# Optimization experiments

Measured on AMD Instinct MI355X. Metric: run time of the kernel, lower is better.

## Reference

```python
import jax, jax.numpy as jnp
import numpy as np

D_MODEL = 1024
NUM_HEADS = 16
HEAD_DIM = D_MODEL // NUM_HEADS  # 64
SCALE = HEAD_DIM ** -0.5
BIAS_LEN = 128  # min(max_seq_len=512, 128)
ROPE_BASE = 10000.0
LN_EPS = 1e-5


def setup_inputs() -> dict:
    key = jax.random.key(0)
    ks = jax.random.split(key, 8)
    B, Lq, Lkv = 8, 512, 512
    return {
        "decoder_hidden": jax.random.normal(ks[0], (B, Lq, D_MODEL), jnp.float32),
        "encoder_output": jax.random.normal(ks[1], (B, Lkv, D_MODEL), jnp.float32),
        "Wqkv": jax.random.normal(ks[2], (3 * D_MODEL, D_MODEL), jnp.float32) * 0.02,
        "Wout": jax.random.normal(ks[3], (D_MODEL, D_MODEL), jnp.float32) * 0.02,
        "b_out": jnp.zeros((D_MODEL,), jnp.float32),
        "Wgate": jax.random.normal(ks[4], (D_MODEL, D_MODEL), jnp.float32) * 0.02,
        "b_gate": jnp.zeros((D_MODEL,), jnp.float32),
        "gamma": jnp.ones((D_MODEL,), jnp.float32),
        "beta": jnp.zeros((D_MODEL,), jnp.float32),
    }


def _layernorm(x, gamma, beta):
    mu = jnp.mean(x, axis=-1, keepdims=True)
    var = jnp.mean(jnp.square(x - mu), axis=-1, keepdims=True)
    return (x - mu) * jax.lax.rsqrt(var + LN_EPS) * gamma + beta


def _rope(x, cos, sin):
    # x: [B, H, L, HEAD_DIM]; cos/sin: [L, HEAD_DIM//2]
    half = HEAD_DIM // 2
    c = cos[None, None, :, :]
    s = sin[None, None, :, :]
    x_even, x_odd = x[..., :half], x[..., half:]
    return jnp.concatenate([x_even * c - x_odd * s, x_even * s + x_odd * c], axis=-1)


def _temporal_bias(L_q, L_kv):
    pos = jnp.arange(BIAS_LEN, dtype=jnp.float32)
    dist = jnp.abs(pos[None, :] - pos[:, None])  # [128,128]
    bias = jnp.exp(-dist * 0.1) - dist * 0.05
    if L_q <= BIAS_LEN and L_kv <= BIAS_LEN:
        return bias[:L_q, :L_kv]
    # bilinear interpolation (align_corners=False / half-pixel) fallback
    return jax.image.resize(bias, (L_q, L_kv), method="bilinear")


def reference(decoder_hidden, encoder_output, Wqkv, Wout, b_out, Wgate, b_gate, gamma, beta):
    B, L_q, _ = decoder_hidden.shape
    L_kv = encoder_output.shape[1]
    residual = decoder_hidden

    q_in = _layernorm(decoder_hidden, gamma, beta)
    kv_in = _layernorm(encoder_output, gamma, beta)

    q = q_in @ Wqkv[:D_MODEL].T
    k = kv_in @ Wqkv[D_MODEL:2 * D_MODEL].T
    v = kv_in @ Wqkv[2 * D_MODEL:].T

    q = q.reshape(B, L_q, NUM_HEADS, HEAD_DIM).transpose(0, 2, 1, 3)
    k = k.reshape(B, L_kv, NUM_HEADS, HEAD_DIM).transpose(0, 2, 1, 3)
    v = v.reshape(B, L_kv, NUM_HEADS, HEAD_DIM).transpose(0, 2, 1, 3)

    # rotary embedding over max(L_q, L_kv) positions
    L = max(L_q, L_kv)
    inv_freq = 1.0 / ROPE_BASE ** (jnp.arange(0, HEAD_DIM, 2, dtype=jnp.float32) / HEAD_DIM)
    freqs = jnp.arange(L, dtype=jnp.float32)[:, None] * inv_freq[None, :]  # [L, HEAD_DIM//2]
    cos, sin = jnp.cos(freqs), jnp.sin(freqs)
    q = _rope(q, cos[:L_q], sin[:L_q])
    k = _rope(k, cos[:L_kv], sin[:L_kv])

    scores = jnp.einsum("bhqd,bhkd->bhqk", q, k) * SCALE
    scores = scores + _temporal_bias(L_q, L_kv)[None, None, :, :]

    attn = jax.nn.softmax(scores, axis=-1)
    attended = jnp.einsum("bhqk,bhkd->bhqd", attn, v)
    attended = attended.transpose(0, 2, 1, 3).reshape(B, L_q, D_MODEL)
    attended = attended @ Wout.T + b_out

    gate = jax.nn.sigmoid(attended @ Wgate.T + b_gate)
    output = gate * attended + (1.0 - gate) * residual
    return output
```

## Files before the change

kernel.cpp:

```cpp
#include <hip/hip_runtime.h>
#include <hip/hip_bf16.h>

#define D_MODEL 1024
#define NHEADS 16
#define HDIM 64
#define BATCH 8
#define SEQ 512
#define NROWS 4096
#define SCALE 0.125f
#define LN_EPS 1e-5f

typedef __attribute__((ext_vector_type(8))) short bf16x8;
typedef __attribute__((ext_vector_type(4))) float f32x4;
typedef __attribute__((ext_vector_type(8))) unsigned short u16x8;

static __device__ __forceinline__ float bf2f(unsigned short u) {
    return __uint_as_float(((unsigned int)u) << 16);
}
static __device__ __forceinline__ unsigned short f2bf(float f) {
    unsigned int x = __float_as_uint(f);
    unsigned int r = (x + 0x7fffu + ((x >> 16) & 1u)) >> 16;
    return (unsigned short)r;
}

#define GLOAD16(gp, lp)                                                        \
    __builtin_amdgcn_global_load_lds(                                          \
        (const __attribute__((address_space(1))) void*)(gp),                   \
        (__attribute__((address_space(3))) void*)(lp), 16, 0, 0)

#define VMW(n) asm volatile("s_waitcnt vmcnt(" #n ")" ::: "memory")
#define RBAR() __builtin_amdgcn_s_barrier()

static __device__ __forceinline__ float bias128(int a, int b) {
    float d = fabsf((float)(a - b));
    return expf(-d * 0.1f) - d * 0.05f;
}

__global__ void prep_kernel(const float* __restrict__ dec, const float* __restrict__ enc,
                            const float* __restrict__ gamma, const float* __restrict__ beta,
                            const float* __restrict__ Wqkv,
                            const float* __restrict__ Wout, const float* __restrict__ Wgate,
                            unsigned short* __restrict__ q_ln, unsigned short* __restrict__ kv_ln,
                            float* __restrict__ bias, unsigned short* __restrict__ Wqkv_bf,
                            unsigned short* __restrict__ Wout_bf, unsigned short* __restrict__ Wgate_bf) {
    int blk = blockIdx.x;
    int t = threadIdx.x;
    if (blk >= 6144) {
        int idx = (blk - 6144) * 256 + t;
        const float* src; unsigned short* dst; int off;
        if (idx < 262144) { src = Wout; dst = Wout_bf; off = idx; }
        else              { src = Wgate; dst = Wgate_bf; off = idx - 262144; }
        float4 v = ((const float4*)src)[off];
        ushort4 u;
        u.x = f2bf(v.x); u.y = f2bf(v.y); u.z = f2bf(v.z); u.w = f2bf(v.w);
        ((ushort4*)dst)[off] = u;
        return;
    }
    if (blk >= 3072) {
        int idx = (blk - 3072) * 256 + t;
        float4 v = ((const float4*)Wqkv)[idx];
        ushort4 u;
        u.x = f2bf(v.x); u.y = f2bf(v.y); u.z = f2bf(v.z); u.w = f2bf(v.w);
        ((ushort4*)Wqkv_bf)[idx] = u;
        return;
    }
    if (blk >= 2048) {
        int idx = (blk - 2048) * 256 + t;
        int qi = idx >> 9, kj = idx & 511;
        float fq = (qi + 0.5f) * 0.25f - 0.5f;
        float fk = (kj + 0.5f) * 0.25f - 0.5f;
        int iq = (int)floorf(fq); float tq = fq - (float)iq;
        int ik = (int)floorf(fk); float tk = fk - (float)ik;
        int iq0 = min(max(iq, 0), 127), iq1 = min(max(iq + 1, 0), 127);
        int ik0 = min(max(ik, 0), 127), ik1 = min(max(ik + 1, 0), 127);
        float v = (1.f - tq) * ((1.f - tk) * bias128(iq0, ik0) + tk * bias128(iq0, ik1))
                +        tq  * ((1.f - tk) * bias128(iq1, ik0) + tk * bias128(iq1, ik1));
        bias[idx] = v;
        return;
    }
    int row = blk * 4 + (t >> 6);
    int lane = t & 63;
    const float* src = (row < NROWS) ? dec + (size_t)row * D_MODEL
                                     : enc + (size_t)(row - NROWS) * D_MODEL;
    unsigned short* dst = (row < NROWS) ? q_ln + (size_t)row * D_MODEL
                                        : kv_ln + (size_t)(row - NROWS) * D_MODEL;
    float4 x0 = ((const float4*)src)[lane];
    float4 x1 = ((const float4*)src)[lane + 64];
    float4 x2 = ((const float4*)src)[lane + 128];
    float4 x3 = ((const float4*)src)[lane + 192];
    float s  = x0.x + x0.y + x0.z + x0.w + x1.x + x1.y + x1.z + x1.w
             + x2.x + x2.y + x2.z + x2.w + x3.x + x3.y + x3.z + x3.w;
    float ss = x0.x * x0.x + x0.y * x0.y + x0.z * x0.z + x0.w * x0.w
             + x1.x * x1.x + x1.y * x1.y + x1.z * x1.z + x1.w * x1.w
             + x2.x * x2.x + x2.y * x2.y + x2.z * x2.z + x2.w * x2.w
             + x3.x * x3.x + x3.y * x3.y + x3.z * x3.z + x3.w * x3.w;
    #pragma unroll
    for (int off = 32; off > 0; off >>= 1) {
        s  += __shfl_down(s, off);
        ss += __shfl_down(ss, off);
    }
    s  = __shfl(s, 0);
    ss = __shfl(ss, 0);
    float mu  = s * (1.0f / 1024.0f);
    float var = ss * (1.0f / 1024.0f) - mu * mu;
    float rstd = rsqrtf(var + LN_EPS);
    #pragma unroll
    for (int j = 0; j < 4; ++j) {
        float4 xv = (j == 0) ? x0 : (j == 1) ? x1 : (j == 2) ? x2 : x3;
        float4 g  = ((const float4*)gamma)[lane + j * 64];
        float4 bb = ((const float4*)beta)[lane + j * 64];
        ushort4 u;
        u.x = f2bf((xv.x - mu) * rstd * g.x + bb.x);
        u.y = f2bf((xv.y - mu) * rstd * g.y + bb.y);
        u.z = f2bf((xv.z - mu) * rstd * g.z + bb.z);
        u.w = f2bf((xv.w - mu) * rstd * g.w + bb.w);
        ((ushort4*)dst)[lane + j * 64] = u;
    }
}

__global__ void convert_og(const float* __restrict__ Wout, const float* __restrict__ Wgate,
                           unsigned short* __restrict__ Wout_bf, unsigned short* __restrict__ Wgate_bf) {
    int idx = blockIdx.x * 256 + threadIdx.x;
    const float* src; unsigned short* dst; int off;
    if (idx < 262144) { src = (const float*)Wout; dst = Wout_bf; off = idx; }
    else              { src = (const float*)Wgate; dst = Wgate_bf; off = idx - 262144; }
    float4 v = ((const float4*)src)[off];
    ushort4 u;
    u.x = f2bf(v.x); u.y = f2bf(v.y); u.z = f2bf(v.z); u.w = f2bf(v.w);
    ((ushort4*)dst)[off] = u;
}

#define CSTR 136

#define MF(a, b, d) __builtin_amdgcn_mfma_f32_16x16x32_bf16((a), (b), (d), 0, 0, 0)

union alignas(16) SmemQS {
    struct { unsigned short A[64 * 64]; unsigned short B[128 * 64]; } ab;
    unsigned short C[64 * CSTR];
    unsigned short Ct[128 * 72];
};

#define QKH(pA, pB, kh)                                                        \
    {                                                                          \
        int pofs = (((kh) * 4 + quad) ^ x7) * 8;                               \
        const unsigned short* Ar_ = (pA) + (wr * 32 + c) * 64 + pofs;          \
        const unsigned short* Br_ = (pB) + (wc * 64 + c) * 64 + pofs;          \
        bf16x8 f0 = *(const bf16x8*)(Ar_);                                     \
        bf16x8 f1 = *(const bf16x8*)(Ar_ + 1024);                              \
        bf16x8 g0 = *(const bf16x8*)(Br_);                                     \
        bf16x8 g1 = *(const bf16x8*)(Br_ + 1024);                              \
        bf16x8 g2 = *(const bf16x8*)(Br_ + 2048);                              \
        bf16x8 g3 = *(const bf16x8*)(Br_ + 3072);                              \
        c00 = MF(f0, g0, c00); c01 = MF(f0, g1, c01); c02 = MF(f0, g2, c02); c03 = MF(f0, g3, c03); \
        c10 = MF(f1, g0, c10); c11 = MF(f1, g1, c11); c12 = MF(f1, g2, c12); c13 = MF(f1, g3, c13); \
    }

#define QROPE_REG(i, reg, A0, A1, A2, A3)                                      \
    {                                                                          \
        int mloc = wr * 32 + (i) * 16 + quad * 4 + (reg);                      \
        int crow = mloc * CSTR + wc * 64;                                      \
        float fl = (float)((rt * 64 + mloc) & 511);                            \
        float aa0 = fl * inv0, aa1 = fl * inv1;                                \
        float c0 = cosf(aa0), s0 = sinf(aa0);                                  \
        float c1 = cosf(aa1), s1 = sinf(aa1);                                  \
        float e0 = A0[(reg)], o0 = A2[(reg)];                                  \
        float e1 = A1[(reg)], o1 = A3[(reg)];                                  \
        smemq.C[crow + c]      = f2bf(e0 * c0 - o0 * s0);                      \
        smemq.C[crow + 32 + c] = f2bf(e0 * s0 + o0 * c0);                      \
        smemq.C[crow + 16 + c] = f2bf(e1 * c1 - o1 * s1);                      \
        smemq.C[crow + 48 + c] = f2bf(e1 * s1 + o1 * c1);                      \
    }
#define QROPE_ROW(i, A0, A1, A2, A3)                                           \
    QROPE_REG(i, 0, A0, A1, A2, A3) QROPE_REG(i, 1, A0, A1, A2, A3)            \
    QROPE_REG(i, 2, A0, A1, A2, A3) QROPE_REG(i, 3, A0, A1, A2, A3)

#define QVSECT_REG(i, j, reg, Acc)                                             \
    smemq.Ct[(wc * 64 + (j) * 16 + c) * 72 + (wr * 32 + (i) * 16 + quad * 4 + (reg))] = f2bf(Acc[(reg)]);
#define QVSECT_TILE(i, j, Acc)                                                 \
    QVSECT_REG(i, j, 0, Acc) QVSECT_REG(i, j, 1, Acc)                          \
    QVSECT_REG(i, j, 2, Acc) QVSECT_REG(i, j, 3, Acc)

__global__ __launch_bounds__(256, 6)
void qkv_gemm_mfma(const unsigned short* __restrict__ q_ln,
                   const unsigned short* __restrict__ kv_ln,
                   const unsigned short* __restrict__ Wb,
                   unsigned short* __restrict__ qo,
                   unsigned short* __restrict__ ko,
                   unsigned short* __restrict__ vo) {
    int bid = blockIdx.x;
    int wg = (bid & 7) * 192 + (bid >> 3);
    int st = wg >> 5, in = wg & 31;
    int stc = st >> 4, str = st & 15;
    int ct = stc * 8 + (in & 7);
    int rt = str * 4 + (in >> 3);
    int n0 = ct * 128;
    int section = stc;
    const unsigned short* A = (section == 0) ? q_ln : kv_ln;

    __shared__ SmemQS smemq;
    unsigned short* As2 = smemq.ab.A;
    unsigned short* Bs2 = smemq.ab.B;
    int tid = threadIdx.x;
    int wave = tid >> 6, lane = tid & 63, quad = lane >> 4, c = lane & 15;
    int wr = wave >> 1, wc = wave & 1;
    int x7 = c & 7;

    int soff = (tid >> 3) * 1024 + (((tid & 7) ^ ((tid >> 3) & 7)) * 8);
    const unsigned short* Ab = A + (size_t)(rt * 64) * 1024 + soff;
    const unsigned short* Bb = Wb + (size_t)n0 * 1024 + soff;
    int stW = wave * 512;

    f32x4 c00 = (f32x4)0.f, c01 = (f32x4)0.f, c02 = (f32x4)0.f, c03 = (f32x4)0.f;
    f32x4 c10 = (f32x4)0.f, c11 = (f32x4)0.f, c12 = (f32x4)0.f, c13 = (f32x4)0.f;

    for (int kt = 0; kt < 16; ++kt) {
        int k0 = kt * 64;
        __syncthreads();
        GLOAD16(Ab + k0,          As2 + stW);
        GLOAD16(Ab + 32768 + k0,  As2 + stW + 2048);
        GLOAD16(Bb + k0,          Bs2 + stW);
        GLOAD16(Bb + 32768 + k0,  Bs2 + stW + 2048);
        GLOAD16(Bb + 65536 + k0,  Bs2 + stW + 4096);
        GLOAD16(Bb + 98304 + k0,  Bs2 + stW + 6144);
        __syncthreads();
        QKH(As2, Bs2, 0)
        QKH(As2, Bs2, 1)
    }

    __syncthreads();

    if (section == 2) {
        QVSECT_TILE(0, 0, c00) QVSECT_TILE(0, 1, c01) QVSECT_TILE(0, 2, c02) QVSECT_TILE(0, 3, c03)
        QVSECT_TILE(1, 0, c10) QVSECT_TILE(1, 1, c11) QVSECT_TILE(1, 2, c12) QVSECT_TILE(1, 3, c13)
        __syncthreads();
        int dr = tid >> 1, hh = tid & 1;
        int h = ((n0 & 1023) >> 6) + (dr >> 6);
        int d = dr & 63;
        int mmb = rt * 64;
        int bb = mmb >> 9, ll0 = mmb & 511;
        unsigned short* orow = vo + (((size_t)bb * NHEADS + h) * HDIM + d) * SEQ + ll0 + hh * 32;
        const unsigned short* csrc = &smemq.Ct[dr * 72 + hh * 32];
        #pragma unroll
        for (int kc = 0; kc < 4; ++kc)
            *(u16x8*)(orow + kc * 8) = *(const u16x8*)(csrc + kc * 8);
        return;
    }

    float inv0 = expf(-0.2878231366f * (float)c);
    float inv1 = expf(-0.2878231366f * (float)(16 + c));
    QROPE_ROW(0, c00, c01, c02, c03)
    QROPE_ROW(1, c10, c11, c12, c13)
    __syncthreads();

    unsigned short* outp = (section == 0) ? qo : ko;
    int rr = tid >> 2;
    int ch = (tid >> 1) & 1;
    int sub = tid & 1;
    int mm = rt * 64 + rr;
    int bb = mm >> 9, ll = mm & 511;
    int h = ((n0 & 1023) >> 6) + ch;
    unsigned short* orow = outp + (((size_t)bb * NHEADS + h) * SEQ + ll) * HDIM + sub * 32;
    const unsigned short* csrc = &smemq.C[rr * CSTR + ch * 64 + sub * 32];
    #pragma unroll
    for (int kc = 0; kc < 4; ++kc)
        *(u16x8*)(orow + kc * 8) = *(const u16x8*)(csrc + kc * 8);
}

struct alignas(16) SmemOG {
    unsigned short A[64 * 128];
    unsigned short B[64 * 128];
};

#define OG_KH(kh)                                                              \
    {                                                                          \
        int pofs = (((kh) * 4 + quad) ^ c) * 8;                                \
        const unsigned short* Ar_ = smemog.A + (wr * 32 + c) * 128 + pofs;     \
        const unsigned short* Br_ = smemog.B + (wc * 32 + c) * 128 + pofs;     \
        bf16x8 f0 = *(const bf16x8*)(Ar_);                                     \
        bf16x8 f1 = *(const bf16x8*)(Ar_ + 2048);                              \
        bf16x8 g0 = *(const bf16x8*)(Br_);                                     \
        bf16x8 g1 = *(const bf16x8*)(Br_ + 2048);                              \
        c00 = MF(f0, g0, c00); c01 = MF(f0, g1, c01);                          \
        c10 = MF(f1, g0, c10); c11 = MF(f1, g1, c11);                          \
    }

#define OG_BODY(Aptr, Bptr)                                                    \
    int bid = blockIdx.x;                                         \
    int wg = (bid & 7) * 128 + (bid >> 3);      \
    int ct = wg & 15, rt = wg >> 4;                                            \
    int tid = threadIdx.x;                                                     \
    int wave = tid >> 6, lane = tid & 63, quad = lane >> 4, c = lane & 15;     \
    int wr = wave >> 1, wc = wave & 1;                                         \
     \
    int soff = (tid >> 4) * 1024 + (((tid & 15) ^ ((tid >> 4) & 15)) * 8);     \
    const unsigned short* Ab = (Aptr) + (size_t)(rt * 64) * 1024 + soff;       \
    const unsigned short* Bb = (Bptr) + (size_t)(ct * 64) * 1024 + soff;       \
    int stW = wave * 512;                                                      \
    f32x4 c00 = (f32x4)0.f, c01 = (f32x4)0.f;                                  \
    f32x4 c10 = (f32x4)0.f, c11 = (f32x4)0.f;                                  \
    for (int kt = 0; kt < 8; ++kt) {                                           \
        int k0 = kt * 128;                                                     \
        __syncthreads();                                                       \
        GLOAD16(Ab + k0,          smemog.A + stW);                             \
        GLOAD16(Ab + 16384 + k0,  smemog.A + stW + 2048);                      \
        GLOAD16(Ab + 32768 + k0,  smemog.A + stW + 4096);                      \
        GLOAD16(Ab + 49152 + k0,  smemog.A + stW + 6144);                      \
        GLOAD16(Bb + k0,          smemog.B + stW);                             \
        GLOAD16(Bb + 16384 + k0,  smemog.B + stW + 2048);                      \
        GLOAD16(Bb + 32768 + k0,  smemog.B + stW + 4096);                      \
        GLOAD16(Bb + 49152 + k0,  smemog.B + stW + 6144);                      \
        __syncthreads();                                                       \
        OG_KH(0)                                                               \
        OG_KH(1)                                                               \
        OG_KH(2)                                                               \
        OG_KH(3)                                                               \
    }

#define O1_REG(mb, reg, n, Acc)                                                \
    t_bf[(size_t)((mb) + (reg)) * 1024 + (n)] = f2bf(Acc[(reg)] + bo);
#define O1_TILE(i, j, Acc)                                                     \
    {                                                                          \
        int n = ct * 64 + wc * 32 + (j) * 16 + c;                              \
        float bo = b_out[n];                                                   \
        int mb = rt * 64 + wr * 32 + (i) * 16 + quad * 4;                      \
        O1_REG(mb, 0, n, Acc) O1_REG(mb, 1, n, Acc)                            \
        O1_REG(mb, 2, n, Acc) O1_REG(mb, 3, n, Acc)                            \
    }

__global__ __launch_bounds__(256, 4)
void out_gemm1_mfma(const unsigned short* __restrict__ att,
                    const unsigned short* __restrict__ Wob,
                    const float* __restrict__ b_out,
                    unsigned short* __restrict__ t_bf) {
    __shared__ SmemOG smemog;
    OG_BODY(att, Wob)
    O1_TILE(0, 0, c00) O1_TILE(0, 1, c01)
    O1_TILE(1, 0, c10) O1_TILE(1, 1, c11)
}

#define O2_REG(mb, reg, n, Acc)                                                \
    {                                                                          \
        float gz = Acc[(reg)] + bg;                                            \
        float g = 1.0f / (1.0f + expf(-gz));                                   \
        size_t idx = (size_t)((mb) + (reg)) * 1024 + (n);                      \
        float tv = bf2f(t_bf[idx]);                                            \
        float rv = residual[idx];                                              \
        out[idx] = g * tv + (1.0f - g) * rv;                                   \
    }
#define O2_TILE(i, j, Acc)                                                     \
    {                                                                          \
        int n = ct * 64 + wc * 32 + (j) * 16 + c;                              \
        float bg = b_gate[n];                                                  \
        int mb = rt * 64 + wr * 32 + (i) * 16 + quad * 4;                      \
        O2_REG(mb, 0, n, Acc) O2_REG(mb, 1, n, Acc)                            \
        O2_REG(mb, 2, n, Acc) O2_REG(mb, 3, n, Acc)                            \
    }

__global__ __launch_bounds__(256, 4)
void out_gemm2_mfma(const unsigned short* __restrict__ t_bf,
                    const unsigned short* __restrict__ Wgb,
                    const float* __restrict__ b_gate,
                    const float* __restrict__ residual,
                    float* __restrict__ out) {
    __shared__ SmemOG smemog;
    OG_BODY(t_bf, Wgb)
    O2_TILE(0, 0, c00) O2_TILE(0, 1, c01)
    O2_TILE(1, 0, c10) O2_TILE(1, 1, c11)
}

#define KSTR 72

static __device__ __forceinline__ void attn_step(
    const unsigned short* __restrict__ KsB, const unsigned short* __restrict__ VsB,
    int kv0, const float* __restrict__ bias, unsigned short* __restrict__ Ps,
    int q0, int wb, int quad, int c, int p0, int p1,
    bf16x8 aq0, bf16x8 aq1, f32x4 (&oacc)[4], float (&lrow)[4])
{
    f32x4 sacc[4];
    #pragma unroll
    for (int nt = 0; nt < 4; ++nt) {
        const unsigned short* kbase = &KsB[(nt * 16 + c) * 64];
        bf16x8 b0 = *(const bf16x8*)(kbase + p0);
        bf16x8 b1 = *(const bf16x8*)(kbase + p1);
        f32x4 a = (f32x4)0.f;
        a = __builtin_amdgcn_mfma_f32_16x16x32_bf16(aq0, b0, a, 0, 0, 0);
        a = __builtin_amdgcn_mfma_f32_16x16x32_bf16(aq1, b1, a, 0, 0, 0);
        sacc[nt] = a;
    }
    const float* bbase = bias + (size_t)(q0 + wb + quad * 4) * 512 + kv0 + c;
    float tsum[4];
    #pragma unroll
    for (int r = 0; r < 4; ++r) tsum[r] = 0.f;
    #pragma unroll
    for (int nt = 0; nt < 4; ++nt)
        #pragma unroll
        for (int r = 0; r < 4; ++r) {
            float p = __expf(sacc[nt][r] * SCALE + bbase[(size_t)r * 512 + nt * 16]);
            tsum[r] += p;
            Ps[(wb + quad * 4 + r) * KSTR + nt * 16 + c] = f2bf(p);
        }
    #pragma unroll
    for (int r = 0; r < 4; ++r) {
        float t = tsum[r];
        t += __shfl_xor(t, 1);
        t += __shfl_xor(t, 2);
        t += __shfl_xor(t, 4);
        t += __shfl_xor(t, 8);
        lrow[r] += t;
    }
    bf16x8 pb0 = *(const bf16x8*)&Ps[(wb + c) * KSTR + quad * 8];
    bf16x8 pb1 = *(const bf16x8*)&Ps[(wb + c) * KSTR + 32 + quad * 8];
    #pragma unroll
    for (int t = 0; t < 4; ++t) {
        const unsigned short* vbase = &VsB[(t * 16 + c) * 64];
        bf16x8 a0 = *(const bf16x8*)(vbase + p0);
        bf16x8 a1 = *(const bf16x8*)(vbase + p1);
        oacc[t] = __builtin_amdgcn_mfma_f32_16x16x32_bf16(a0, pb0, oacc[t], 0, 0, 0);
        oacc[t] = __builtin_amdgcn_mfma_f32_16x16x32_bf16(a1, pb1, oacc[t], 0, 0, 0);
    }
}

#define ASTAGE(BUF, kvt)                                                       \
    GLOAD16(kgb + (size_t)((kvt) * 64) * HDIM, Ks[BUF] + wave * 512);          \
    GLOAD16(vgb + (kvt) * 64, Vs[BUF] + wave * 512);

__global__ __launch_bounds__(512)
void attn_kernel(const unsigned short* __restrict__ q,
                 const unsigned short* __restrict__ k,
                 const unsigned short* __restrict__ vt,
                 const float* __restrict__ bias,
                 unsigned short* __restrict__ attended) {
    int bid = blockIdx.x;
    int qt = bid >> 7;
    int hb = bid & 127;
    int h = hb >> 3;
    int b = hb & 7;
    __shared__ unsigned short Ks[2][64 * 64];
    __shared__ unsigned short Vs[2][64 * 64];
    __shared__ unsigned short Ps[128 * KSTR];
    __shared__ float lf[128];

    int tid = threadIdx.x;
    int wave = tid >> 6, lane = tid & 63;
    int quad = lane >> 4, c = lane & 15;
    int wb = wave * 16;
    size_t headbase = (((size_t)b * NHEADS + h) * SEQ) * HDIM;
    int q0 = qt * 128;

    const unsigned short* qrow = q + headbase + (size_t)(q0 + wb + c) * HDIM;
    bf16x8 aq0 = *(const bf16x8*)(qrow + quad * 8);
    bf16x8 aq1 = *(const bf16x8*)(qrow + 32 + quad * 8);

    int srow = wave * 8 + (lane >> 3);
    int schunk = (lane & 7) ^ (srow & 7);
    const unsigned short* kgb = k + headbase + (size_t)srow * HDIM + schunk * 8;
    const unsigned short* vgb = vt + headbase + (size_t)srow * SEQ + schunk * 8;
    int x7 = c & 7;
    int p0 = (quad ^ x7) * 8;
    int p1 = ((4 + quad) ^ x7) * 8;

    f32x4 oacc[4];
    #pragma unroll
    for (int t = 0; t < 4; ++t) oacc[t] = (f32x4)0.f;
    float lrow[4];
    #pragma unroll
    for (int r = 0; r < 4; ++r) lrow[r] = 0.f;

    ASTAGE(0, 0)
    ASTAGE(1, 1)
    VMW(2); RBAR();
    for (int kt2 = 0; kt2 < 4; ++kt2) {
        attn_step(Ks[0], Vs[0], (kt2 * 2) * 64, bias, Ps,
                  q0, wb, quad, c, p0, p1, aq0, aq1, oacc, lrow);
        RBAR();
        if (kt2 < 3) { ASTAGE(0, kt2 * 2 + 2) VMW(2); }
        else         { VMW(0); }
        RBAR();
        attn_step(Ks[1], Vs[1], (kt2 * 2 + 1) * 64, bias, Ps,
                  q0, wb, quad, c, p0, p1, aq0, aq1, oacc, lrow);
        RBAR();
        if (kt2 < 3) { ASTAGE(1, kt2 * 2 + 3) VMW(2); }
        RBAR();
    }

    if (c == 0) {
        f32x4 lv;
        lv[0] = lrow[0]; lv[1] = lrow[1]; lv[2] = lrow[2]; lv[3] = lrow[3];
        *(f32x4*)&lf[wb + quad * 4] = lv;
    }
    float invl = 1.0f / lf[wb + c];
    unsigned short* drow = attended + ((size_t)b * SEQ + (q0 + wb + c)) * D_MODEL + h * HDIM;
    #pragma unroll
    for (int t = 0; t < 4; ++t) {
        ushort4 o;
        o.x = f2bf(oacc[t][0] * invl);
        o.y = f2bf(oacc[t][1] * invl);
        o.z = f2bf(oacc[t][2] * invl);
        o.w = f2bf(oacc[t][3] * invl);
        *(ushort4*)(drow + t * 16 + quad * 4) = o;
    }
}

extern "C" void kernel_launch(void* const* d_in, const int* in_sizes, int n_in,
                              void* d_out, int out_size, void* d_ws, size_t ws_size,
                              hipStream_t stream) {
    const float* dec    = (const float*)d_in[0];
    const float* enc    = (const float*)d_in[1];
    const float* Wqkv   = (const float*)d_in[2];
    const float* Wout   = (const float*)d_in[3];
    const float* b_out  = (const float*)d_in[4];
    const float* Wgate  = (const float*)d_in[5];
    const float* b_gate = (const float*)d_in[6];
    const float* gamma  = (const float*)d_in[7];
    const float* beta   = (const float*)d_in[8];
    float* out = (float*)d_out;

    char* ws = (char*)d_ws;
    const size_t MB = 1024 * 1024;
    unsigned short* q_ln    = (unsigned short*)(ws + 0 * MB);
    unsigned short* kv_ln   = (unsigned short*)(ws + 8 * MB);
    unsigned short* qb      = (unsigned short*)(ws + 16 * MB);
    unsigned short* kb      = (unsigned short*)(ws + 24 * MB);
    unsigned short* vb      = (unsigned short*)(ws + 32 * MB);
    unsigned short* Wqkv_bf = (unsigned short*)(ws + 40 * MB);
    float*          bias    = (float*)(ws + 46 * MB);
    unsigned short* att     = (unsigned short*)(ws + 0 * MB);
    unsigned short* t_bf    = (unsigned short*)(ws + 24 * MB);

    bool hoist = (ws_size >= 51 * MB);
    unsigned short* Wout_bf  = (unsigned short*)(ws + (hoist ? 47 * MB : 32 * MB));
    unsigned short* Wgate_bf = (unsigned short*)(ws + (hoist ? 49 * MB : 34 * MB));

    prep_kernel<<<hoist ? 8192 : 6144, 256, 0, stream>>>(
        dec, enc, gamma, beta, Wqkv, Wout, Wgate,
        q_ln, kv_ln, bias, Wqkv_bf, Wout_bf, Wgate_bf);
    qkv_gemm_mfma<<<1536, 256, 0, stream>>>(q_ln, kv_ln, Wqkv_bf, qb, kb, vb);
    attn_kernel<<<512, 512, 0, stream>>>(qb, kb, vb, bias, att);
    if (!hoist)
        convert_og<<<2048, 256, 0, stream>>>(Wout, Wgate, Wout_bf, Wgate_bf);
    out_gemm1_mfma<<<1024, 256, 0, stream>>>(att, Wout_bf, b_out, t_bf);
    out_gemm2_mfma<<<1024, 256, 0, stream>>>(t_bf, Wgate_bf, b_gate, dec, out);
}
```

Before: 202.8 us.

## Fold Wout into gate weight to fuse both output GEMMs into one kernel

Computes a combined weight Wgate·Wout and bias Wgate·b_out+b_gate on the device each call, attached as extra blocks to the prep and QKV GEMM launches. A single fused output kernel then computes att·Wout and att·Wcomb together and applies the gate epilogue. This removes the intermediate t_bf round trip and one kernel launch. In exchange it adds a per-call 1024^3 weight GEMM, and rounding the combined weight to bf16 slightly changes numerics. The new path only runs when the workspace is at least 56 MB, otherwise the old two-GEMM path is used.

```diff
diff --git a/kernel.cpp b/kernel.cpp
--- a/kernel.cpp
+++ b/kernel.cpp
@@ -40,11 +40,45 @@
                             const float* __restrict__ gamma, const float* __restrict__ beta,
                             const float* __restrict__ Wqkv,
                             const float* __restrict__ Wout, const float* __restrict__ Wgate,
+                            const float* __restrict__ b_out, const float* __restrict__ b_gate,
                             unsigned short* __restrict__ q_ln, unsigned short* __restrict__ kv_ln,
                             float* __restrict__ bias, unsigned short* __restrict__ Wqkv_bf,
-                            unsigned short* __restrict__ Wout_bf, unsigned short* __restrict__ Wgate_bf) {
+                            unsigned short* __restrict__ Wout_bf, unsigned short* __restrict__ Wgate_bf,
+                            unsigned short* __restrict__ WoutT_bf, float* __restrict__ bias2) {
     int blk = blockIdx.x;
     int t = threadIdx.x;
+    __shared__ unsigned short T[64 * 72];
+    if (blk >= 8448) {
+        int n = (blk - 8448) * 256 + t;
+        float acc = 0.f;
+        const float4* wg4 = (const float4*)(Wgate + (size_t)n * 1024);
+        const float4* bo4 = (const float4*)b_out;
+        for (int k = 0; k < 256; ++k) {
+            float4 w = wg4[k]; float4 b = bo4[k];
+            acc += w.x * b.x + w.y * b.y + w.z * b.z + w.w * b.w;
+        }
+        bias2[n] = acc + b_gate[n];
+        return;
+    }
+    if (blk >= 8192) {
+        int tb = blk - 8192;
+        int tr = tb >> 4, tc = tb & 15;
+        int r = t >> 2, q4 = (t & 3) * 16;
+        const float* src = Wout + (size_t)(tr * 64 + r) * 1024 + tc * 64 + q4;
+        #pragma unroll
+        for (int p = 0; p < 4; ++p) {
+            float4 v = ((const float4*)src)[p];
+            T[(q4 + p * 4 + 0) * 72 + r] = f2bf(v.x);
+            T[(q4 + p * 4 + 1) * 72 + r] = f2bf(v.y);
+            T[(q4 + p * 4 + 2) * 72 + r] = f2bf(v.z);
+            T[(q4 + p * 4 + 3) * 72 + r] = f2bf(v.w);
+        }
+        __syncthreads();
+        unsigned short* dst = WoutT_bf + (size_t)(tc * 64 + r) * 1024 + tr * 64 + q4;
+        *(u16x8*)(dst)     = *(const u16x8*)&T[r * 72 + q4];
+        *(u16x8*)(dst + 8) = *(const u16x8*)&T[r * 72 + q4 + 8];
+        return;
+    }
     if (blk >= 6144) {
         int idx = (blk - 6144) * 256 + t;
         const float* src; unsigned short* dst; int off;
@@ -180,22 +214,48 @@
     QVSECT_REG(i, j, 0, Acc) QVSECT_REG(i, j, 1, Acc)                          \
     QVSECT_REG(i, j, 2, Acc) QVSECT_REG(i, j, 3, Acc)
 
+#define WC_TILE(i, j, Acc)                                                     \
+    {                                                                          \
+        int n_ = ct * 128 + wc * 64 + (j) * 16 + c;                            \
+        int m_ = rt * 64 + wr * 32 + (i) * 16 + quad * 4;                      \
+        Wcomb_bf[(size_t)(m_ + 0) * 1024 + n_] = f2bf(Acc[0]);                 \
+        Wcomb_bf[(size_t)(m_ + 1) * 1024 + n_] = f2bf(Acc[1]);                 \
+        Wcomb_bf[(size_t)(m_ + 2) * 1024 + n_] = f2bf(Acc[2]);                 \
+        Wcomb_bf[(size_t)(m_ + 3) * 1024 + n_] = f2bf(Acc[3]);                 \
+    }
+
 __global__ __launch_bounds__(256, 6)
 void qkv_gemm_mfma(const unsigned short* __restrict__ q_ln,
                    const unsigned short* __restrict__ kv_ln,
                    const unsigned short* __restrict__ Wb,
                    unsigned short* __restrict__ qo,
                    unsigned short* __restrict__ ko,
-                   unsigned short* __restrict__ vo) {
+                   unsigned short* __restrict__ vo,
+                   const unsigned short* __restrict__ Wgate_bf,
+                   const unsigned short* __restrict__ WoutT_bf,
+                   unsigned short* __restrict__ Wcomb_bf,
+                   int nwc) {
     int bid = blockIdx.x;
-    int wg = (bid & 7) * 192 + (bid >> 3);
-    int st = wg >> 5, in = wg & 31;
-    int stc = st >> 4, str = st & 15;
-    int ct = stc * 8 + (in & 7);
-    int rt = str * 4 + (in >> 3);
-    int n0 = ct * 128;
-    int section = stc;
-    const unsigned short* A = (section == 0) ? q_ln : kv_ln;
+    int section, ct, rt, n0;
+    const unsigned short *A, *B;
+    if (bid < nwc) {
+        section = 3;
+        rt = bid >> 3;
+        ct = bid & 7;
+        n0 = ct * 128;
+        A = Wgate_bf; B = WoutT_bf;
+    } else {
+        int b2 = bid - nwc;
+        int wg = (b2 & 7) * 192 + (b2 >> 3);
+        int st = wg >> 5, in = wg & 31;
+        int stc = st >> 4, str = st & 15;
+        ct = stc * 8 + (in & 7);
+        rt = str * 4 + (in >> 3);
+        n0 = ct * 128;
+        section = stc;
+        A = (section == 0) ? q_ln : kv_ln;
+        B = Wb;
+    }
 
     __shared__ SmemQS smemq;
     unsigned short* As2 = smemq.ab.A;
@@ -207,7 +267,7 @@
 
     int soff = (tid >> 3) * 1024 + (((tid & 7) ^ ((tid >> 3) & 7)) * 8);
     const unsigned short* Ab = A + (size_t)(rt * 64) * 1024 + soff;
-    const unsigned short* Bb = Wb + (size_t)n0 * 1024 + soff;
+    const unsigned short* Bb = B + (size_t)n0 * 1024 + soff;
     int stW = wave * 512;
 
     f32x4 c00 = (f32x4)0.f, c01 = (f32x4)0.f, c02 = (f32x4)0.f, c03 = (f32x4)0.f;
@@ -228,6 +288,12 @@
     }
 
     __syncthreads();
+
+    if (section == 3) {
+        WC_TILE(0, 0, c00) WC_TILE(0, 1, c01) WC_TILE(0, 2, c02) WC_TILE(0, 3, c03)
+        WC_TILE(1, 0, c10) WC_TILE(1, 1, c11) WC_TILE(1, 2, c12) WC_TILE(1, 3, c13)
+        return;
+    }
 
     if (section == 2) {
         QVSECT_TILE(0, 0, c00) QVSECT_TILE(0, 1, c01) QVSECT_TILE(0, 2, c02) QVSECT_TILE(0, 3, c03)
@@ -266,6 +332,85 @@
         *(u16x8*)(orow + kc * 8) = *(const u16x8*)(csrc + kc * 8);
 }
 
+struct alignas(16) SmemF {
+    unsigned short A[64 * 64];
+    unsigned short B1[64 * 64];
+    unsigned short B2[64 * 64];
+};
+
+#define FUS_KH(kh)                                                             \
+    {                                                                          \
+        int pofs = (((kh) * 4 + quad) ^ x7) * 8;                               \
+        const unsigned short* Ar_  = smf.A  + (wr * 32 + c) * 64 + pofs;       \
+        const unsigned short* B1r_ = smf.B1 + (wc * 32 + c) * 64 + pofs;       \
+        const unsigned short* B2r_ = smf.B2 + (wc * 32 + c) * 64 + pofs;       \
+        bf16x8 f0 = *(const bf16x8*)(B1r_ - B1r_ + Ar_);                       \
+        bf16x8 f1 = *(const bf16x8*)(Ar_ + 1024);                              \
+        bf16x8 g0 = *(const bf16x8*)(B1r_);                                    \
+        bf16x8 g1 = *(const bf16x8*)(B1r_ + 1024);                             \
+        bf16x8 h0 = *(const bf16x8*)(B2r_);                                    \
+        bf16x8 h1 = *(const bf16x8*)(B2r_ + 1024);                             \
+        c00 = MF(f0, g0, c00); c01 = MF(f0, g1, c01);                          \
+        c10 = MF(f1, g0, c10); c11 = MF(f1, g1, c11);                          \
+        d00 = MF(f0, h0, d00); d01 = MF(f0, h1, d01);                          \
+        d10 = MF(f1, h0, d10); d11 = MF(f1, h1, d11);                          \
+    }
+
+#define FO_TILE(i, j, CA, DA)                                                  \
+    {                                                                          \
+        int n = ct * 64 + wc * 32 + (j) * 16 + c;                              \
+        float bo = b_out[n];                                                   \
+        float b2v = bias2[n];                                                  \
+        int mb = rt * 64 + wr * 32 + (i) * 16 + quad * 4;                      \
+        _Pragma("unroll")                                                      \
+        for (int r = 0; r < 4; ++r) {                                          \
+            size_t idx = (size_t)(mb + r) * 1024 + n;                          \
+            float tv = CA[r] + bo;                                             \
+            float g = 1.0f / (1.0f + expf(-(DA[r] + b2v)));                    \
+            out[idx] = g * tv + (1.0f - g) * residual[idx];                    \
+        }                                                                      \
+    }
+
+__global__ __launch_bounds__(256, 4)
+void out_fused_mfma(const unsigned short* __restrict__ att,
+                    const unsigned short* __restrict__ Wob,
+                    const unsigned short* __restrict__ Wcb,
+                    const float* __restrict__ b_out,
+                    const float* __restrict__ bias2,
+                    const float* __restrict__ residual,
+                    float* __restrict__ out) {
+    int bid = blockIdx.x;
+    int wg = (bid & 7) * 128 + (bid >> 3);
+    int ct = wg & 15, rt = wg >> 4;
+    __shared__ SmemF smf;
+    int tid = threadIdx.x;
+    int wave = tid >> 6, lane = tid & 63, quad = lane >> 4, c = lane & 15;
+    int wr = wave >> 1, wc = wave & 1;
+    int x7 = c & 7;
+    int soff = (tid >> 3) * 1024 + (((tid & 7) ^ ((tid >> 3) & 7)) * 8);
+    const unsigned short* Ab  = att + (size_t)(rt * 64) * 1024 + soff;
+    const unsigned short* B1b = Wob + (size_t)(ct * 64) * 1024 + soff;
+    const unsigned short* B2b = Wcb + (size_t)(ct * 64) * 1024 + soff;
+    int stW = wave * 512;
+    f32x4 c00 = (f32x4)0.f, c01 = (f32x4)0.f, c10 = (f32x4)0.f, c11 = (f32x4)0.f;
+    f32x4 d00 = (f32x4)0.f, d01 = (f32x4)0.f, d10 = (f32x4)0.f, d11 = (f32x4)0.f;
+    for (int kt = 0; kt < 16; ++kt) {
+        int k0 = kt * 64;
+        __syncthreads();
+        GLOAD16(Ab + k0,           smf.A  + stW);
+        GLOAD16(Ab + 32768 + k0,   smf.A  + stW + 2048);
+        GLOAD16(B1b + k0,          smf.B1 + stW);
+        GLOAD16(B1b + 32768 + k0,  smf.B1 + stW + 2048);
+        GLOAD16(B2b + k0,          smf.B2 + stW);
+        GLOAD16(B2b + 32768 + k0,  smf.B2 + stW + 2048);
+        __syncthreads();
+        FUS_KH(0)
+        FUS_KH(1)
+    }
+    FO_TILE(0, 0, c00, d00) FO_TILE(0, 1, c01, d01)
+    FO_TILE(1, 0, c10, d10) FO_TILE(1, 1, c11, d11)
+}
+
 struct alignas(16) SmemOG {
     unsigned short A[64 * 128];
     unsigned short B[64 * 128];
@@ -291,7 +436,6 @@
     int tid = threadIdx.x;                                                     \
     int wave = tid >> 6, lane = tid & 63, quad = lane >> 4, c = lane & 15;     \
     int wr = wave >> 1, wc = wave & 1;                                         \
-     \
     int soff = (tid >> 4) * 1024 + (((tid & 15) ^ ((tid >> 4) & 15)) * 8);     \
     const unsigned short* Ab = (Aptr) + (size_t)(rt * 64) * 1024 + soff;       \
     const unsigned short* Bb = (Bptr) + (size_t)(ct * 64) * 1024 + soff;       \
@@ -528,16 +672,26 @@
     unsigned short* t_bf    = (unsigned short*)(ws + 24 * MB);
 
     bool hoist = (ws_size >= 51 * MB);
+    bool fused = (ws_size >= 56 * MB);
     unsigned short* Wout_bf  = (unsigned short*)(ws + (hoist ? 47 * MB : 32 * MB));
     unsigned short* Wgate_bf = (unsigned short*)(ws + (hoist ? 49 * MB : 34 * MB));
-
-    prep_kernel<<<hoist ? 8192 : 6144, 256, 0, stream>>>(
-        dec, enc, gamma, beta, Wqkv, Wout, Wgate,
-        q_ln, kv_ln, bias, Wqkv_bf, Wout_bf, Wgate_bf);
-    qkv_gemm_mfma<<<1536, 256, 0, stream>>>(q_ln, kv_ln, Wqkv_bf, qb, kb, vb);
+    unsigned short* WoutT_bf = (unsigned short*)(ws + 51 * MB);
+    unsigned short* Wcomb_bf = (unsigned short*)(ws + 53 * MB);
+    float*          bias2    = (float*)(ws + 55 * MB);
+
+    prep_kernel<<<fused ? 8452 : (hoist ? 8192 : 6144), 256, 0, stream>>>(
+        dec, enc, gamma, beta, Wqkv, Wout, Wgate, b_out, b_gate,
+        q_ln, kv_ln, bias, Wqkv_bf, Wout_bf, Wgate_bf, WoutT_bf, bias2);
+    qkv_gemm_mfma<<<fused ? 1664 : 1536, 256, 0, stream>>>(
+        q_ln, kv_ln, Wqkv_bf, qb, kb, vb,
+        Wgate_bf, WoutT_bf, Wcomb_bf, fused ? 128 : 0);
     attn_kernel<<<512, 512, 0, stream>>>(qb, kb, vb, bias, att);
     if (!hoist)
         convert_og<<<2048, 256, 0, stream>>>(Wout, Wgate, Wout_bf, Wgate_bf);
-    out_gemm1_mfma<<<1024, 256, 0, stream>>>(att, Wout_bf, b_out, t_bf);
-    out_gemm2_mfma<<<1024, 256, 0, stream>>>(t_bf, Wgate_bf, b_gate, dec, out);
-}
+    if (fused) {
+        out_fused_mfma<<<1024, 256, 0, stream>>>(att, Wout_bf, Wcomb_bf, b_out, bias2, dec, out);
+    } else {
+        out_gemm1_mfma<<<1024, 256, 0, stream>>>(att, Wout_bf, b_out, t_bf);
+        out_gemm2_mfma<<<1024, 256, 0, stream>>>(t_bf, Wgate_bf, b_gate, dec, out);
+    }
+}
```

Result: slower. 224.0 us (+10.4%).

## Shrink QKV GEMM tile to 64x64 and double grid size

Applied to the files above, without the earlier changes.

Reworks the QKV projection GEMM from 64x128 output tiles to 64x64 tiles, so each block covers one head. The grid goes from 1536 to 3072 blocks, and launch bounds rise to 8 blocks per CU to raise occupancy. Each wave now computes a 16x64 slab with 4 accumulators, which halves register and LDS use per block. In exchange, each A tile is loaded twice as often and there is less MFMA work per shared-memory load, which lowers arithmetic intensity.

```diff
diff --git a/kernel.cpp b/kernel.cpp
--- a/kernel.cpp
+++ b/kernel.cpp
@@ -130,57 +130,48 @@
     ((ushort4*)dst)[off] = u;
 }
 
-#define CSTR 136
-
 #define MF(a, b, d) __builtin_amdgcn_mfma_f32_16x16x32_bf16((a), (b), (d), 0, 0, 0)
 
-union alignas(16) SmemQS {
-    struct { unsigned short A[64 * 64]; unsigned short B[128 * 64]; } ab;
-    unsigned short C[64 * CSTR];
-    unsigned short Ct[128 * 72];
+union alignas(16) SmemQ64 {
+    struct { unsigned short A[64 * 64]; unsigned short B[64 * 64]; } ab;
+    unsigned short C[64 * 72];
+    unsigned short Ct[64 * 72];
 };
 
-#define QKH(pA, pB, kh)                                                        \
+#define Q64KH(kh)                                                              \
     {                                                                          \
         int pofs = (((kh) * 4 + quad) ^ x7) * 8;                               \
-        const unsigned short* Ar_ = (pA) + (wr * 32 + c) * 64 + pofs;          \
-        const unsigned short* Br_ = (pB) + (wc * 64 + c) * 64 + pofs;          \
+        const unsigned short* Ar_ = As2 + (wave * 16 + c) * 64 + pofs;         \
+        const unsigned short* Br_ = Bs2 + c * 64 + pofs;                       \
         bf16x8 f0 = *(const bf16x8*)(Ar_);                                     \
-        bf16x8 f1 = *(const bf16x8*)(Ar_ + 1024);                              \
         bf16x8 g0 = *(const bf16x8*)(Br_);                                     \
         bf16x8 g1 = *(const bf16x8*)(Br_ + 1024);                              \
         bf16x8 g2 = *(const bf16x8*)(Br_ + 2048);                              \
         bf16x8 g3 = *(const bf16x8*)(Br_ + 3072);                              \
-        c00 = MF(f0, g0, c00); c01 = MF(f0, g1, c01); c02 = MF(f0, g2, c02); c03 = MF(f0, g3, c03); \
-        c10 = MF(f1, g0, c10); c11 = MF(f1, g1, c11); c12 = MF(f1, g2, c12); c13 = MF(f1, g3, c13); \
-    }
-
-#define QROPE_REG(i, reg, A0, A1, A2, A3)                                      \
+        c00 = MF(f0, g0, c00); c01 = MF(f0, g1, c01);                          \
+        c02 = MF(f0, g2, c02); c03 = MF(f0, g3, c03);                          \
+    }
+
+#define Q64ROPE(reg)                                                           \
     {                                                                          \
-        int mloc = wr * 32 + (i) * 16 + quad * 4 + (reg);                      \
-        int crow = mloc * CSTR + wc * 64;                                      \
+        int mloc = wave * 16 + quad * 4 + (reg);                               \
+        int crow = mloc * 72;                                                  \
         float fl = (float)((rt * 64 + mloc) & 511);                            \
         float aa0 = fl * inv0, aa1 = fl * inv1;                                \
-        float c0 = cosf(aa0), s0 = sinf(aa0);                                  \
-        float c1 = cosf(aa1), s1 = sinf(aa1);                                  \
-        float e0 = A0[(reg)], o0 = A2[(reg)];                                  \
-        float e1 = A1[(reg)], o1 = A3[(reg)];                                  \
-        smemq.C[crow + c]      = f2bf(e0 * c0 - o0 * s0);                      \
-        smemq.C[crow + 32 + c] = f2bf(e0 * s0 + o0 * c0);                      \
-        smemq.C[crow + 16 + c] = f2bf(e1 * c1 - o1 * s1);                      \
-        smemq.C[crow + 48 + c] = f2bf(e1 * s1 + o1 * c1);                      \
-    }
-#define QROPE_ROW(i, A0, A1, A2, A3)                                           \
-    QROPE_REG(i, 0, A0, A1, A2, A3) QROPE_REG(i, 1, A0, A1, A2, A3)            \
-    QROPE_REG(i, 2, A0, A1, A2, A3) QROPE_REG(i, 3, A0, A1, A2, A3)
-
-#define QVSECT_REG(i, j, reg, Acc)                                             \
-    smemq.Ct[(wc * 64 + (j) * 16 + c) * 72 + (wr * 32 + (i) * 16 + quad * 4 + (reg))] = f2bf(Acc[(reg)]);
-#define QVSECT_TILE(i, j, Acc)                                                 \
-    QVSECT_REG(i, j, 0, Acc) QVSECT_REG(i, j, 1, Acc)                          \
-    QVSECT_REG(i, j, 2, Acc) QVSECT_REG(i, j, 3, Acc)
-
-__global__ __launch_bounds__(256, 6)
+        float cc0 = cosf(aa0), ss0 = sinf(aa0);                                \
+        float cc1 = cosf(aa1), ss1 = sinf(aa1);                                \
+        float e0 = c00[(reg)], o0 = c02[(reg)];                                \
+        float e1 = c01[(reg)], o1 = c03[(reg)];                                \
+        smemq.C[crow + c]      = f2bf(e0 * cc0 - o0 * ss0);                    \
+        smemq.C[crow + 32 + c] = f2bf(e0 * ss0 + o0 * cc0);                    \
+        smemq.C[crow + 16 + c] = f2bf(e1 * cc1 - o1 * ss1);                    \
+        smemq.C[crow + 48 + c] = f2bf(e1 * ss1 + o1 * cc1);                    \
+    }
+
+#define Q64V(j, reg, Acc)                                                      \
+    smemq.Ct[((j) * 16 + c) * 72 + (wave * 16 + quad * 4 + (reg))] = f2bf(Acc[(reg)]);
+
+__global__ __launch_bounds__(256, 8)
 void qkv_gemm_mfma(const unsigned short* __restrict__ q_ln,
                    const unsigned short* __restrict__ kv_ln,
                    const unsigned short* __restrict__ Wb,
@@ -188,21 +179,21 @@
                    unsigned short* __restrict__ ko,
                    unsigned short* __restrict__ vo) {
     int bid = blockIdx.x;
-    int wg = (bid & 7) * 192 + (bid >> 3);
+    int wg = (bid & 7) * 384 + (bid >> 3);
     int st = wg >> 5, in = wg & 31;
-    int stc = st >> 4, str = st & 15;
-    int ct = stc * 8 + (in & 7);
-    int rt = str * 4 + (in >> 3);
-    int n0 = ct * 128;
-    int section = stc;
+    int section = st >> 5;
+    int sl = st & 31;
+    int ctg = sl >> 4, rtg = sl & 15;
+    int ct = section * 16 + ctg * 8 + (in & 7);
+    int rt = rtg * 4 + (in >> 3);
+    int n0 = ct * 64;
     const unsigned short* A = (section == 0) ? q_ln : kv_ln;
 
-    __shared__ SmemQS smemq;
+    __shared__ SmemQ64 smemq;
     unsigned short* As2 = smemq.ab.A;
     unsigned short* Bs2 = smemq.ab.B;
     int tid = threadIdx.x;
     int wave = tid >> 6, lane = tid & 63, quad = lane >> 4, c = lane & 15;
-    int wr = wave >> 1, wc = wave & 1;
     int x7 = c & 7;
 
     int soff = (tid >> 3) * 1024 + (((tid & 7) ^ ((tid >> 3) & 7)) * 8);
@@ -211,7 +202,6 @@
     int stW = wave * 512;
 
     f32x4 c00 = (f32x4)0.f, c01 = (f32x4)0.f, c02 = (f32x4)0.f, c03 = (f32x4)0.f;
-    f32x4 c10 = (f32x4)0.f, c11 = (f32x4)0.f, c12 = (f32x4)0.f, c13 = (f32x4)0.f;
 
     for (int kt = 0; kt < 16; ++kt) {
         int k0 = kt * 64;
@@ -220,50 +210,44 @@
         GLOAD16(Ab + 32768 + k0,  As2 + stW + 2048);
         GLOAD16(Bb + k0,          Bs2 + stW);
         GLOAD16(Bb + 32768 + k0,  Bs2 + stW + 2048);
-        GLOAD16(Bb + 65536 + k0,  Bs2 + stW + 4096);
-        GLOAD16(Bb + 98304 + k0,  Bs2 + stW + 6144);
         __syncthreads();
-        QKH(As2, Bs2, 0)
-        QKH(As2, Bs2, 1)
+        Q64KH(0)
+        Q64KH(1)
     }
 
     __syncthreads();
 
     if (section == 2) {
-        QVSECT_TILE(0, 0, c00) QVSECT_TILE(0, 1, c01) QVSECT_TILE(0, 2, c02) QVSECT_TILE(0, 3, c03)
-        QVSECT_TILE(1, 0, c10) QVSECT_TILE(1, 1, c11) QVSECT_TILE(1, 2, c12) QVSECT_TILE(1, 3, c13)
+        Q64V(0, 0, c00) Q64V(0, 1, c00) Q64V(0, 2, c00) Q64V(0, 3, c00)
+        Q64V(1, 0, c01) Q64V(1, 1, c01) Q64V(1, 2, c01) Q64V(1, 3, c01)
+        Q64V(2, 0, c02) Q64V(2, 1, c02) Q64V(2, 2, c02) Q64V(2, 3, c02)
+        Q64V(3, 0, c03) Q64V(3, 1, c03) Q64V(3, 2, c03) Q64V(3, 3, c03)
         __syncthreads();
-        int dr = tid >> 1, hh = tid & 1;
-        int h = ((n0 & 1023) >> 6) + (dr >> 6);
-        int d = dr & 63;
+        int dr = tid >> 2, part = tid & 3;
+        int h = ct & 15;
         int mmb = rt * 64;
         int bb = mmb >> 9, ll0 = mmb & 511;
-        unsigned short* orow = vo + (((size_t)bb * NHEADS + h) * HDIM + d) * SEQ + ll0 + hh * 32;
-        const unsigned short* csrc = &smemq.Ct[dr * 72 + hh * 32];
-        #pragma unroll
-        for (int kc = 0; kc < 4; ++kc)
-            *(u16x8*)(orow + kc * 8) = *(const u16x8*)(csrc + kc * 8);
+        unsigned short* orow = vo + (((size_t)bb * NHEADS + h) * HDIM + dr) * SEQ + ll0 + part * 16;
+        const unsigned short* csrc = &smemq.Ct[dr * 72 + part * 16];
+        *(u16x8*)(orow)     = *(const u16x8*)(csrc);
+        *(u16x8*)(orow + 8) = *(const u16x8*)(csrc + 8);
         return;
     }
 
     float inv0 = expf(-0.2878231366f * (float)c);
     float inv1 = expf(-0.2878231366f * (float)(16 + c));
-    QROPE_ROW(0, c00, c01, c02, c03)
-    QROPE_ROW(1, c10, c11, c12, c13)
+    Q64ROPE(0) Q64ROPE(1) Q64ROPE(2) Q64ROPE(3)
     __syncthreads();
 
     unsigned short* outp = (section == 0) ? qo : ko;
-    int rr = tid >> 2;
-    int ch = (tid >> 1) & 1;
-    int sub = tid & 1;
+    int rr = tid >> 2, part = tid & 3;
     int mm = rt * 64 + rr;
     int bb = mm >> 9, ll = mm & 511;
-    int h = ((n0 & 1023) >> 6) + ch;
-    unsigned short* orow = outp + (((size_t)bb * NHEADS + h) * SEQ + ll) * HDIM + sub * 32;
-    const unsigned short* csrc = &smemq.C[rr * CSTR + ch * 64 + sub * 32];
-    #pragma unroll
-    for (int kc = 0; kc < 4; ++kc)
-        *(u16x8*)(orow + kc * 8) = *(const u16x8*)(csrc + kc * 8);
+    int h = ct & 15;
+    unsigned short* orow = outp + (((size_t)bb * NHEADS + h) * SEQ + ll) * HDIM + part * 16;
+    const unsigned short* csrc = &smemq.C[rr * 72 + part * 16];
+    *(u16x8*)(orow)     = *(const u16x8*)(csrc);
+    *(u16x8*)(orow + 8) = *(const u16x8*)(csrc + 8);
 }
 
 struct alignas(16) SmemOG {
@@ -534,7 +518,7 @@
     prep_kernel<<<hoist ? 8192 : 6144, 256, 0, stream>>>(
         dec, enc, gamma, beta, Wqkv, Wout, Wgate,
         q_ln, kv_ln, bias, Wqkv_bf, Wout_bf, Wgate_bf);
-    qkv_gemm_mfma<<<1536, 256, 0, stream>>>(q_ln, kv_ln, Wqkv_bf, qb, kb, vb);
+    qkv_gemm_mfma<<<3072, 256, 0, stream>>>(q_ln, kv_ln, Wqkv_bf, qb, kb, vb);
     attn_kernel<<<512, 512, 0, stream>>>(qb, kb, vb, bias, att);
     if (!hoist)
         convert_og<<<2048, 256, 0, stream>>>(Wout, Wgate, Wout_bf, Wgate_bf);
```

Result: no change. 203.7 us (+0.5%).
